# Optimization experiments

Measured on AMD Instinct MI355X. Metric: run time of the kernel, lower is better.

The kernel has to match this reference:

```python
import jax, jax.numpy as jnp
import numpy as np

B, C, IMG, P = 64, 3, 224, 16
GRID = IMG // P          # 14
N = GRID * GRID          # 196 patch tokens
D = 768
L, H = 12, 12
HD = D // H              # 64
FF = 4 * D               # 3072
NC = 1000
PRUNE_LAYER = 6
KEEP = max(1, int(N * 0.5))  # 98 tokens kept after pruning
LN_EPS = 1e-6


def _ln(x, g, b):
    m = jnp.mean(x, axis=-1, keepdims=True)
    v = jnp.var(x, axis=-1, keepdims=True)
    return (x - m) * jax.lax.rsqrt(v + LN_EPS) * g + b


def _block(x, g1, b1, qw, qb, pw, pb, g2, b2, w1, c1, w2, c2):
    # standard timm ViT block: x + Attn(LN(x)); x + MLP(LN(x))
    Bq, S, _ = x.shape
    h = _ln(x, g1, b1)
    qkv = (h @ qw + qb).reshape(Bq, S, 3, H, HD)
    q, k, v = qkv[:, :, 0], qkv[:, :, 1], qkv[:, :, 2]  # [B,S,H,HD]
    attn = jax.nn.softmax(jnp.einsum('bqhd,bkhd->bhqk', q, k) * (HD ** -0.5), axis=-1)
    o = jnp.einsum('bhqk,bkhd->bqhd', attn, v).reshape(Bq, S, D)
    x = x + o @ pw + pb
    h = _ln(x, g2, b2)
    return x + jax.nn.gelu(h @ w1 + c1, approximate=False) @ w2 + c2


def _forward(x, patch_w, patch_b, cls_token, pos_embed, ln1_g, ln1_b, qkv_w, qkv_b,
             proj_w, proj_b, ln2_g, ln2_b, fc1_w, fc1_b, fc2_w, fc2_b,
             norm_g, norm_b, head_w, head_b):
    Bq = x.shape[0]
    # patch embed: conv(k=16, s=16) == patchify + linear; flatten order (C, ph, pw) matches torch conv weight layout
    patches = x.reshape(Bq, C, GRID, P, GRID, P).transpose(0, 2, 4, 1, 3, 5).reshape(Bq, N, C * P * P)
    t = patches @ patch_w + patch_b                                     # [B,N,D]
    t = jnp.concatenate([jnp.broadcast_to(cls_token, (Bq, 1, D)), t], axis=1) + pos_embed  # [B,197,D]

    blk = lambda t, i: _block(t, ln1_g[i], ln1_b[i], qkv_w[i], qkv_b[i], proj_w[i], proj_b[i],
                              ln2_g[i], ln2_b[i], fc1_w[i], fc1_b[i], fc2_w[i], fc2_b[i])
    for i in range(PRUNE_LAYER):
        t = blk(t, i)

    cls_tok, patch_tok = t[:, :1], t[:, 1:]
    # per-token L2 scores + topk selection + gather (the irregular-access stage)
    scores = jnp.sqrt(jnp.sum(patch_tok * patch_tok, axis=-1))          # [B,N]
    _, idx = jax.lax.top_k(scores, KEEP)                                # sorted descending, matches torch.topk
    sel = jnp.take_along_axis(patch_tok, idx[:, :, None], axis=1)       # [B,K,D]
    t = jnp.concatenate([cls_tok, sel], axis=1)                         # [B,K+1,D]

    for i in range(PRUNE_LAYER, L):
        t = blk(t, i)
    t = _ln(t, norm_g, norm_b)
    return t[:, 0] @ head_w + head_b                                    # [B,NC]


def setup_inputs() -> dict:
    key = jax.random.key(0)
    ks = jax.random.split(key, 12)
    s = 0.02
    f32 = jnp.float32
    return {
        'x': jax.random.normal(ks[0], (B, C, IMG, IMG), f32),
        'patch_w': jax.random.normal(ks[1], (C * P * P, D), f32) * s,
        'patch_b': jnp.zeros((D,), f32),
        'cls_token': jax.random.normal(ks[2], (1, 1, D), f32) * s,
        'pos_embed': jax.random.normal(ks[3], (1, N + 1, D), f32) * s,
        'ln1_g': jnp.ones((L, D), f32), 'ln1_b': jnp.zeros((L, D), f32),
        'qkv_w': jax.random.normal(ks[4], (L, D, 3 * D), f32) * s,
        'qkv_b': jnp.zeros((L, 3 * D), f32),
        'proj_w': jax.random.normal(ks[5], (L, D, D), f32) * s,
        'proj_b': jnp.zeros((L, D), f32),
        'ln2_g': jnp.ones((L, D), f32), 'ln2_b': jnp.zeros((L, D), f32),
        'fc1_w': jax.random.normal(ks[6], (L, D, FF), f32) * s,
        'fc1_b': jnp.zeros((L, FF), f32),
        'fc2_w': jax.random.normal(ks[7], (L, FF, D), f32) * s,
        'fc2_b': jnp.zeros((L, D), f32),
        'norm_g': jnp.ones((D,), f32), 'norm_b': jnp.zeros((D,), f32),
        'head_w': jax.random.normal(ks[8], (D, NC), f32) * s,
        'head_b': jnp.zeros((NC,), f32),
    }


def reference(x, patch_w, patch_b, cls_token, pos_embed, ln1_g, ln1_b, qkv_w, qkv_b,
              proj_w, proj_b, ln2_g, ln2_b, fc1_w, fc1_b, fc2_w, fc2_b,
              norm_g, norm_b, head_w, head_b):
    return _forward(x, patch_w, patch_b, cls_token, pos_embed, ln1_g, ln1_b, qkv_w, qkv_b,
                    proj_w, proj_b, ln2_g, ln2_b, fc1_w, fc1_b, fc2_w, fc2_b,
                    norm_g, norm_b, head_w, head_b)
```

## Files before the change

kernel.cpp:

```cpp
#include <hip/hip_runtime.h>
#include <hip/hip_bf16.h>
#include <cstddef>
#include <cstdint>

namespace {

constexpr int B = 64, CIN = 3, IMG = 224, PS = 16, GRID_ = 14, NPATCH = 196;
constexpr int D = 768, H = 12, HD = 64, FFD = 3072, NC = 1000;
constexpr int S1 = 197, S2 = 99, KEEP = 98, PRUNE = 6, LAYERS = 12;
constexpr float LN_EPS = 1e-6f;

typedef __attribute__((ext_vector_type(8))) short bf16x8;
typedef __attribute__((ext_vector_type(4))) float f32x4;

__device__ inline float wave_red_sum(float v) {
  #pragma unroll
  for (int off = 32; off > 0; off >>= 1) v += __shfl_xor(v, off, 64);
  return v;
}

__device__ inline void gl16(const __hip_bfloat16* g, __hip_bfloat16* l) {
  __builtin_amdgcn_global_load_lds(
      (const __attribute__((address_space(1))) void*)g,
      (__attribute__((address_space(3))) void*)l,
      16, 0, 0);
}

__global__ __launch_bounds__(256) void tcvt_k(const float* __restrict__ src,
                                              __hip_bfloat16* __restrict__ dst,
                                              int R, int C, size_t lstride) {
  src += (size_t)blockIdx.z * lstride;
  dst += (size_t)blockIdx.z * lstride;
  __shared__ float tile[32][33];
  int c0 = blockIdx.x * 32, r0 = blockIdx.y * 32;
  int tx = threadIdx.x & 31, ty = threadIdx.x >> 5;
  #pragma unroll
  for (int i = 0; i < 32; i += 8) {
    int r = r0 + ty + i, c = c0 + tx;
    tile[ty + i][tx] = (r < R && c < C) ? src[(size_t)r * C + c] : 0.f;
  }
  __syncthreads();
  #pragma unroll
  for (int i = 0; i < 32; i += 8) {
    int c = c0 + ty + i, r = r0 + tx;
    if (c < C && r < R) dst[(size_t)c * R + r] = __float2bfloat16(tile[tx][ty + i]);
  }
}

__global__ void patchify_k(const float* __restrict__ x, __hip_bfloat16* __restrict__ out) {
  size_t idx = (size_t)blockIdx.x * blockDim.x + threadIdx.x;
  size_t total = (size_t)B * NPATCH * D;
  if (idx >= total) return;
  int row = (int)(idx / D), k = (int)(idx % D);
  int b = row / NPATCH, n = row % NPATCH;
  int gr = n / GRID_, gc = n % GRID_;
  int c = k / (PS * PS), rr = (k % (PS * PS)) / PS, cc = k % PS;
  out[idx] = __float2bfloat16(x[((size_t)(b * CIN + c) * IMG + (gr * PS + rr)) * IMG + gc * PS + cc]);
}

template <int MODE, int KC>
__global__ __launch_bounds__(256) void bgemm_k(
    const __hip_bfloat16* __restrict__ A, const __hip_bfloat16* __restrict__ BT,
    const float* __restrict__ bias, void* __restrict__ Cc,
    int M, int N, const float* __restrict__ extra) {
  __shared__ __hip_bfloat16 As[3][128 * 32];
  __shared__ __hip_bfloat16 Bs[3][128 * 32];
  int tid = threadIdx.x, lane = tid & 63, wv = tid >> 6;
  int wr = wv >> 1, wc = wv & 1;

  int nbx = gridDim.x, nby = gridDim.y;
  int nwg = nbx * nby;
  int flat = blockIdx.y * nbx + blockIdx.x;
  int q8 = nwg >> 3, r8 = nwg & 7;
  int xcd = flat & 7, pos = flat >> 3;
  int nf = (xcd < r8 ? xcd * (q8 + 1) : r8 * (q8 + 1) + (xcd - r8) * q8) + pos;
  constexpr int G = 8;
  int fullS = nby / G, tailR = nby - fullS * G;
  int fullCount = fullS * G * nbx;
  int bx, by;
  if (nf < fullCount) {
    int sup = nf / (G * nbx);
    int rem = nf - sup * G * nbx;
    bx = rem / G;
    by = sup * G + (rem - bx * G);
  } else {
    int rem = nf - fullCount;
    bx = rem / tailR;
    by = fullS * G + (rem - bx * tailR);
  }
  int m0 = by * 128, n0 = bx * 128;

  int fr = lane & 15, fq = lane >> 4;
  int srow = lane >> 2;
  int scd = (lane & 3) ^ ((lane >> 3) & 3);
  int rswz = (fq ^ ((fr >> 1) & 3)) * 8;
  constexpr int NK = KC >> 5;

  int r0i = m0 + wv * 32 + srow, r1i = r0i + 16;
  int ga0 = (r0i < M) ? r0i : (M - 1), ga1 = (r1i < M) ? r1i : (M - 1);
  int c0i = n0 + wv * 32 + srow, c1i = c0i + 16;
  int gb0 = (c0i < N) ? c0i : (N - 1), gb1 = (c1i < N) ? c1i : (N - 1);
  const __hip_bfloat16* pa0 = A + (size_t)ga0 * KC + scd * 8;
  const __hip_bfloat16* pa1 = A + (size_t)ga1 * KC + scd * 8;
  const __hip_bfloat16* pb0 = BT + (size_t)gb0 * KC + scd * 8;
  const __hip_bfloat16* pb1 = BT + (size_t)gb1 * KC + scd * 8;

  auto stage = [&](int buf, int kt) {
    int ko = kt << 5;
    gl16(pa0 + ko, &As[buf][(wv * 32) * 32]);
    gl16(pa1 + ko, &As[buf][(wv * 32 + 16) * 32]);
    gl16(pb0 + ko, &Bs[buf][(wv * 32) * 32]);
    gl16(pb1 + ko, &Bs[buf][(wv * 32 + 16) * 32]);
  };

  f32x4 acc[4][4] = {};
  stage(0, 0);
  stage(1, 1);
  #pragma unroll 4
  for (int kt = 0; kt < NK; ++kt) {
    int buf = kt % 3;
    if (kt + 2 < NK) {
      stage((kt + 2) % 3, kt + 2);
      asm volatile("s_waitcnt vmcnt(8)" ::: "memory");
    } else if (kt + 1 < NK) {
      asm volatile("s_waitcnt vmcnt(4)" ::: "memory");
    } else {
      asm volatile("s_waitcnt vmcnt(0)" ::: "memory");
    }
    asm volatile("s_barrier" ::: "memory");
    bf16x8 af[4], bg[4];
    #pragma unroll
    for (int m = 0; m < 4; ++m)
      af[m] = *(const bf16x8*)&As[buf][(wr * 64 + m * 16 + fr) * 32 + rswz];
    #pragma unroll
    for (int n = 0; n < 4; ++n)
      bg[n] = *(const bf16x8*)&Bs[buf][(wc * 64 + n * 16 + fr) * 32 + rswz];
    #pragma unroll
    for (int m = 0; m < 4; ++m)
      #pragma unroll
      for (int n = 0; n < 4; ++n)
        acc[m][n] = __builtin_amdgcn_mfma_f32_16x16x32_bf16(af[m], bg[n], acc[m][n], 0, 0, 0);
    asm volatile("s_waitcnt lgkmcnt(0)" ::: "memory");
    asm volatile("s_barrier" ::: "memory");
  }
  #pragma unroll
  for (int m = 0; m < 4; ++m) {
    #pragma unroll
    for (int n = 0; n < 4; ++n) {
      #pragma unroll
      for (int j = 0; j < 4; ++j) {
        int row = m0 + wr * 64 + m * 16 + fq * 4 + j;
        int col = n0 + wc * 64 + n * 16 + fr;
        if (row >= M || col >= N) continue;
        float v = acc[m][n][j] + bias[col];
        if (MODE == 0) {
          ((__hip_bfloat16*)Cc)[(size_t)row * N + col] = __float2bfloat16(v);
        } else if (MODE == 1) {
          int b = row / NPATCH, nn = row % NPATCH;
          ((float*)Cc)[((size_t)(b * S1 + 1 + nn)) * D + col] = v + extra[(size_t)(1 + nn) * D + col];
        } else if (MODE == 2) {
          ((float*)Cc)[(size_t)row * N + col] += v;
        } else {
          float g = 0.5f * v * (1.0f + erff(v * 0.7071067811865476f));
          ((__hip_bfloat16*)Cc)[(size_t)row * N + col] = __float2bfloat16(g);
        }
      }
    }
  }
}

__global__ __launch_bounds__(256) void gemm_k(
    const float* __restrict__ A, const float* __restrict__ Bw,
    const float* __restrict__ bias, float* __restrict__ Cc,
    int M, int N, int K) {
  __shared__ float As[64][17];
  __shared__ float Bs[16][64];
  int tid = threadIdx.x;
  int tx = tid & 15, ty = tid >> 4;
  int m0 = blockIdx.y * 64, n0 = blockIdx.x * 64;
  float acc[4][4] = {};
  for (int k0 = 0; k0 < K; k0 += 16) {
    #pragma unroll
    for (int j = 0; j < 4; ++j) {
      int i = tid + 256 * j;
      int r = i >> 4, c = i & 15;
      int gr = m0 + r;
      As[r][c] = (gr < M) ? A[(size_t)gr * K + (k0 + c)] : 0.f;
    }
    #pragma unroll
    for (int j = 0; j < 4; ++j) {
      int i = tid + 256 * j;
      int r = i >> 6, c = i & 63;
      int gc = n0 + c;
      Bs[r][c] = (gc < N) ? Bw[(size_t)(k0 + r) * N + gc] : 0.f;
    }
    __syncthreads();
    #pragma unroll
    for (int kk = 0; kk < 16; ++kk) {
      float a[4], bb[4];
      #pragma unroll
      for (int ii = 0; ii < 4; ++ii) a[ii] = As[ty * 4 + ii][kk];
      #pragma unroll
      for (int jj = 0; jj < 4; ++jj) bb[jj] = Bs[kk][tx * 4 + jj];
      #pragma unroll
      for (int ii = 0; ii < 4; ++ii)
        #pragma unroll
        for (int jj = 0; jj < 4; ++jj) acc[ii][jj] = fmaf(a[ii], bb[jj], acc[ii][jj]);
    }
    __syncthreads();
  }
  #pragma unroll
  for (int ii = 0; ii < 4; ++ii) {
    int row = m0 + ty * 4 + ii;
    if (row >= M) continue;
    #pragma unroll
    for (int jj = 0; jj < 4; ++jj) {
      int col = n0 + tx * 4 + jj;
      if (col >= N) continue;
      Cc[(size_t)row * N + col] = acc[ii][jj] + bias[col];
    }
  }
}

__global__ void cls_init_k(float* __restrict__ t, const float* __restrict__ cls,
                           const float* __restrict__ pos) {
  int idx = blockIdx.x * blockDim.x + threadIdx.x;
  if (idx >= B * D) return;
  int b = idx / D, d = idx % D;
  t[(size_t)b * S1 * D + d] = cls[d] + pos[d];
}

template <typename OutT>
__global__ __launch_bounds__(192) void ln_k(const float* __restrict__ in, OutT* __restrict__ out,
                                            const float* __restrict__ g, const float* __restrict__ bta,
                                            size_t istride, size_t ostride) {
  int row = blockIdx.x, tid = threadIdx.x;
  const float4* p = (const float4*)(in + (size_t)row * istride);
  float4 v = p[tid];
  float s = v.x + v.y + v.z + v.w;
  float s2 = v.x * v.x + v.y * v.y + v.z * v.z + v.w * v.w;
  s = wave_red_sum(s);
  s2 = wave_red_sum(s2);
  __shared__ float r1[3], r2[3];
  int lane = tid & 63, w = tid >> 6;
  if (lane == 0) { r1[w] = s; r2[w] = s2; }
  __syncthreads();
  s = r1[0] + r1[1] + r1[2];
  s2 = r2[0] + r2[1] + r2[2];
  float mean = s * (1.0f / 768.0f);
  float var = s2 * (1.0f / 768.0f) - mean * mean;
  float rs = rsqrtf(var + LN_EPS);
  float4 gv = ((const float4*)g)[tid];
  float4 bv = ((const float4*)bta)[tid];
  float o0 = (v.x - mean) * rs * gv.x + bv.x;
  float o1 = (v.y - mean) * rs * gv.y + bv.y;
  float o2 = (v.z - mean) * rs * gv.z + bv.z;
  float o3 = (v.w - mean) * rs * gv.w + bv.w;
  if constexpr (sizeof(OutT) == 2) {
    __hip_bfloat16 hb[4] = {__float2bfloat16(o0), __float2bfloat16(o1),
                            __float2bfloat16(o2), __float2bfloat16(o3)};
    *(uint2*)((__hip_bfloat16*)out + (size_t)row * ostride + tid * 4) = *(uint2*)hb;
  } else {
    ((float4*)((float*)out + (size_t)row * ostride))[tid] = make_float4(o0, o1, o2, o3);
  }
}

template <int NT16>
__global__ __launch_bounds__(256) void attn3_k(const __hip_bfloat16* __restrict__ qkv,
                                               __hip_bfloat16* __restrict__ o, int S) {
  constexpr int NT32 = (NT16 + 1) / 2;
  constexpr int COLS = NT32 * 32;
  constexpr int STR = COLS + 8;
  __shared__ __hip_bfloat16 VT[64 * STR];
  __shared__ __hip_bfloat16 P[4][16 * STR];
  int bh = blockIdx.x;
  int b = bh / H, hh = bh % H;
  int tid = threadIdx.x, lane = tid & 63, wv = tid >> 6;
  int fr = lane & 15, fq = lane >> 4;
  const size_t rs = 3 * D;
  const __hip_bfloat16* qb = qkv + ((size_t)b * S) * rs + hh * HD;
  const __hip_bfloat16* kb = qb + D;
  const __hip_bfloat16* vb = qb + 2 * D;
  const __hip_bfloat16 z = __float2bfloat16(0.f);
  for (int idx = tid; idx < COLS * 64; idx += 256) {
    int key = idx >> 6, d = idx & 63;
    VT[d * STR + key] = (key < S) ? vb[(size_t)key * rs + d] : z;
  }
  if (NT16 & 1) {
    for (int idx = lane; idx < 16 * 16; idx += 64)
      P[wv][(idx >> 4) * STR + NT16 * 16 + (idx & 15)] = z;
  }
  __syncthreads();

  for (int qt = wv; qt * 16 < S; qt += 4) {
    int q0 = qt * 16;
    int qrow = q0 + fr;
    const __hip_bfloat16* qp = qb + (size_t)(qrow < S ? qrow : 0) * rs + fq * 8;
    bf16x8 aq0 = *(const bf16x8*)(qp);
    bf16x8 aq1 = *(const bf16x8*)(qp + 32);
    f32x4 sc[NT16];
    #pragma unroll
    for (int kt = 0; kt < NT16; ++kt) {
      int krow = kt * 16 + fr;
      const __hip_bfloat16* kp = kb + (size_t)(krow < S ? krow : 0) * rs + fq * 8;
      bf16x8 bk0 = *(const bf16x8*)(kp);
      bf16x8 bk1 = *(const bf16x8*)(kp + 32);
      f32x4 a = {};
      a = __builtin_amdgcn_mfma_f32_16x16x32_bf16(aq0, bk0, a, 0, 0, 0);
      a = __builtin_amdgcn_mfma_f32_16x16x32_bf16(aq1, bk1, a, 0, 0, 0);
      sc[kt] = a;
    }
    float lj[4];
    #pragma unroll
    for (int jj = 0; jj < 4; ++jj) {
      float mx = -1e30f;
      #pragma unroll
      for (int kt = 0; kt < NT16; ++kt) {
        float v = sc[kt][jj] * 0.125f;
        if (kt * 16 + fr >= S) v = -1e30f;
        sc[kt][jj] = v;
        mx = fmaxf(mx, v);
      }
      mx = fmaxf(mx, __shfl_xor(mx, 1, 64));
      mx = fmaxf(mx, __shfl_xor(mx, 2, 64));
      mx = fmaxf(mx, __shfl_xor(mx, 4, 64));
      mx = fmaxf(mx, __shfl_xor(mx, 8, 64));
      float sum = 0.f;
      #pragma unroll
      for (int kt = 0; kt < NT16; ++kt) {
        float p = __expf(sc[kt][jj] - mx);
        sc[kt][jj] = p;
        sum += p;
      }
      sum += __shfl_xor(sum, 1, 64);
      sum += __shfl_xor(sum, 2, 64);
      sum += __shfl_xor(sum, 4, 64);
      sum += __shfl_xor(sum, 8, 64);
      lj[jj] = 1.0f / sum;
    }
    __hip_bfloat16* pw = &P[wv][0];
    #pragma unroll
    for (int kt = 0; kt < NT16; ++kt)
      #pragma unroll
      for (int jj = 0; jj < 4; ++jj)
        pw[(fq * 4 + jj) * STR + kt * 16 + fr] = __float2bfloat16(sc[kt][jj]);
    #pragma unroll
    for (int dt = 0; dt < 4; ++dt) {
      f32x4 oa = {};
      #pragma unroll
      for (int kc = 0; kc < NT32; ++kc) {
        bf16x8 ap = *(const bf16x8*)&pw[fr * STR + kc * 32 + fq * 8];
        bf16x8 bv = *(const bf16x8*)&VT[(dt * 16 + fr) * STR + kc * 32 + fq * 8];
        oa = __builtin_amdgcn_mfma_f32_16x16x32_bf16(ap, bv, oa, 0, 0, 0);
      }
      #pragma unroll
      for (int jj = 0; jj < 4; ++jj) {
        int orow = q0 + fq * 4 + jj;
        if (orow < S)
          o[((size_t)(b * S + orow)) * D + hh * HD + dt * 16 + fr] =
              __float2bfloat16(oa[jj] * lj[jj]);
      }
    }
  }
}

__global__ void score_k(const float* __restrict__ t, float* __restrict__ scores) {
  int gw = (blockIdx.x * blockDim.x + threadIdx.x) >> 6;
  int lane = threadIdx.x & 63;
  if (gw >= B * NPATCH) return;
  int b = gw / NPATCH, n = gw % NPATCH;
  const float* p = t + ((size_t)(b * S1) + 1 + n) * D;
  float a = 0.f;
  #pragma unroll
  for (int j = lane; j < D; j += 64) { float v = p[j]; a += v * v; }
  a = wave_red_sum(a);
  if (lane == 0) scores[gw] = sqrtf(a);
}

__global__ __launch_bounds__(256) void select_k(const float* __restrict__ scores, int* __restrict__ map) {
  int b = blockIdx.x;
  __shared__ float s[NPATCH];
  __shared__ int flag[NPATCH];
  int i = threadIdx.x;
  if (i < NPATCH) s[i] = scores[b * NPATCH + i];
  __syncthreads();
  if (i < NPATCH) {
    float si = s[i];
    int r = 0;
    for (int j = 0; j < NPATCH; ++j) {
      float sj = s[j];
      r += (sj > si) || (sj == si && j < i);
    }
    flag[i] = (r < KEEP) ? 1 : 0;
  }
  __syncthreads();
  if (i < NPATCH && flag[i]) {
    int p = 0;
    for (int j = 0; j < i; ++j) p += flag[j];
    map[b * (KEEP + 1) + 1 + p] = 1 + i;
  }
  if (i == 0) map[b * (KEEP + 1)] = 0;
}

__global__ void gather_k(const float* __restrict__ t, const int* __restrict__ map,
                         float* __restrict__ t2) {
  int br = blockIdx.x;
  int b = br / S2;
  int src = map[br];
  const float* p = t + ((size_t)b * S1 + src) * D;
  float* q = t2 + (size_t)br * D;
  for (int j = threadIdx.x; j < D; j += blockDim.x) q[j] = p[j];
}

}

extern "C" void kernel_launch(void* const* d_in, const int* in_sizes, int n_in,
                              void* d_out, int out_size, void* d_ws, size_t ws_size,
                              hipStream_t stream) {
  const float* x       = (const float*)d_in[0];
  const float* patch_w = (const float*)d_in[1];
  const float* patch_b = (const float*)d_in[2];
  const float* cls_tok = (const float*)d_in[3];
  const float* pos_emb = (const float*)d_in[4];
  const float* ln1_g   = (const float*)d_in[5];
  const float* ln1_b   = (const float*)d_in[6];
  const float* qkv_w   = (const float*)d_in[7];
  const float* qkv_b   = (const float*)d_in[8];
  const float* proj_w  = (const float*)d_in[9];
  const float* proj_b  = (const float*)d_in[10];
  const float* ln2_g   = (const float*)d_in[11];
  const float* ln2_b   = (const float*)d_in[12];
  const float* fc1_w   = (const float*)d_in[13];
  const float* fc1_b   = (const float*)d_in[14];
  const float* fc2_w   = (const float*)d_in[15];
  const float* fc2_b   = (const float*)d_in[16];
  const float* norm_g  = (const float*)d_in[17];
  const float* norm_b  = (const float*)d_in[18];
  const float* head_w  = (const float*)d_in[19];
  const float* head_b  = (const float*)d_in[20];
  float* out = (float*)d_out;

  char* wp = (char*)d_ws;
  auto alloc = [&](size_t bytes) { char* r = wp; wp += (bytes + 255) & ~(size_t)255; return r; };
  float* t   = (float*)alloc((size_t)B * S1 * D * 4);
  float* t2  = (float*)alloc((size_t)B * S2 * D * 4);
  float* hf  = (float*)alloc((size_t)B * D * 4);
  float* scores = (float*)alloc((size_t)B * NPATCH * 4);
  int*   map    = (int*)alloc((size_t)B * S2 * 4);
  __hip_bfloat16* h   = (__hip_bfloat16*)alloc((size_t)B * S1 * D * 2);
  __hip_bfloat16* qkv = (__hip_bfloat16*)alloc((size_t)B * S1 * 3 * D * 2);
  __hip_bfloat16* ff  = (__hip_bfloat16*)alloc((size_t)B * S1 * FFD * 2);
  __hip_bfloat16* qkvT  = (__hip_bfloat16*)alloc((size_t)LAYERS * 3 * D * D * 2);
  __hip_bfloat16* projT = (__hip_bfloat16*)alloc((size_t)LAYERS * D * D * 2);
  __hip_bfloat16* fc1T  = (__hip_bfloat16*)alloc((size_t)LAYERS * FFD * D * 2);
  __hip_bfloat16* fc2T  = (__hip_bfloat16*)alloc((size_t)LAYERS * D * FFD * 2);
  __hip_bfloat16* patchT = (__hip_bfloat16*)alloc((size_t)D * D * 2);
  __hip_bfloat16* patches = ff;

  { dim3 g(3 * D / 32, D / 32, LAYERS);
    tcvt_k<<<g, 256, 0, stream>>>(qkv_w, qkvT, D, 3 * D, (size_t)D * 3 * D); }
  { dim3 g(D / 32, D / 32, LAYERS);
    tcvt_k<<<g, 256, 0, stream>>>(proj_w, projT, D, D, (size_t)D * D); }
  { dim3 g(FFD / 32, D / 32, LAYERS);
    tcvt_k<<<g, 256, 0, stream>>>(fc1_w, fc1T, D, FFD, (size_t)D * FFD); }
  { dim3 g(D / 32, FFD / 32, LAYERS);
    tcvt_k<<<g, 256, 0, stream>>>(fc2_w, fc2T, FFD, D, (size_t)FFD * D); }
  { dim3 g(D / 32, D / 32, 1);
    tcvt_k<<<g, 256, 0, stream>>>(patch_w, patchT, D, D, 0); }

  {
    size_t total = (size_t)B * NPATCH * D;
    patchify_k<<<(unsigned)((total + 255) / 256), 256, 0, stream>>>(x, patches);
    dim3 g(D / 128, (B * NPATCH) / 128);
    bgemm_k<1, 768><<<g, 256, 0, stream>>>(patches, patchT, patch_b, t, B * NPATCH, D, pos_emb);
    cls_init_k<<<(B * D + 255) / 256, 256, 0, stream>>>(t, cls_tok, pos_emb);
  }

  auto run_block = [&](float* tb, int S, int l) {
    int M = B * S;
    int mb = (M + 127) / 128;
    ln_k<__hip_bfloat16><<<M, 192, 0, stream>>>(tb, h, ln1_g + (size_t)l * D, ln1_b + (size_t)l * D, D, D);
    { dim3 g(3 * D / 128, mb);
      bgemm_k<0, 768><<<g, 256, 0, stream>>>(h, qkvT + (size_t)l * 3 * D * D, qkv_b + (size_t)l * 3 * D,
                                             qkv, M, 3 * D, nullptr); }
    if (S == S1) attn3_k<13><<<B * H, 256, 0, stream>>>(qkv, h, S);
    else         attn3_k<7><<<B * H, 256, 0, stream>>>(qkv, h, S);
    { dim3 g(D / 128, mb);
      bgemm_k<2, 768><<<g, 256, 0, stream>>>(h, projT + (size_t)l * D * D, proj_b + (size_t)l * D,
                                             tb, M, D, nullptr); }
    ln_k<__hip_bfloat16><<<M, 192, 0, stream>>>(tb, h, ln2_g + (size_t)l * D, ln2_b + (size_t)l * D, D, D);
    { dim3 g(FFD / 128, mb);
      bgemm_k<3, 768><<<g, 256, 0, stream>>>(h, fc1T + (size_t)l * FFD * D, fc1_b + (size_t)l * FFD,
                                             ff, M, FFD, nullptr); }
    { dim3 g(D / 128, mb);
      bgemm_k<2, 3072><<<g, 256, 0, stream>>>(ff, fc2T + (size_t)l * D * FFD, fc2_b + (size_t)l * D,
                                              tb, M, D, nullptr); }
  };

  for (int l = 0; l < PRUNE; ++l) run_block(t, S1, l);

  score_k<<<(B * NPATCH * 64 + 255) / 256, 256, 0, stream>>>(t, scores);
  select_k<<<B, 256, 0, stream>>>(scores, map);
  gather_k<<<B * S2, 256, 0, stream>>>(t, map, t2);

  for (int l = PRUNE; l < LAYERS; ++l) run_block(t2, S2, l);

  ln_k<float><<<B, 192, 0, stream>>>(t2, hf, norm_g, norm_b, (size_t)S2 * D, D);
  { dim3 g((NC + 63) / 64, (B + 63) / 64);
    gemm_k<<<g, 256, 0, stream>>>(hf, head_w, head_b, out, B, NC, D); }
}
```

Before: 5.778 ms.

## Add 64-row GEMM tile variant for narrow-N GEMMs and drop XCD swizzle

Templates the bf16 MFMA GEMM on the M tile height (128 or 64) and uses 64-row tiles for the proj GEMM and the post-prune fc2 GEMM, where N=768 gives only six column tiles. The smaller tile doubles the workgroup count to fill more CUs, at the cost of less B-tile reuse per workgroup. It also removes the XCD-aware grouped block remapping, which can hurt L2 locality, and drops the unroll-4 pragma on the k loop.

```diff
diff --git a/kernel.cpp b/kernel.cpp
--- a/kernel.cpp
+++ b/kernel.cpp
@@ -58,85 +58,74 @@
   out[idx] = __float2bfloat16(x[((size_t)(b * CIN + c) * IMG + (gr * PS + rr)) * IMG + gc * PS + cc]);
 }
 
-template <int MODE, int KC>
+template <int MODE, int KC, int BM>
 __global__ __launch_bounds__(256) void bgemm_k(
     const __hip_bfloat16* __restrict__ A, const __hip_bfloat16* __restrict__ BT,
     const float* __restrict__ bias, void* __restrict__ Cc,
     int M, int N, const float* __restrict__ extra) {
-  __shared__ __hip_bfloat16 As[3][128 * 32];
+  constexpr int MR = BM / 32;
+  __shared__ __hip_bfloat16 As[3][BM * 32];
   __shared__ __hip_bfloat16 Bs[3][128 * 32];
   int tid = threadIdx.x, lane = tid & 63, wv = tid >> 6;
   int wr = wv >> 1, wc = wv & 1;
-
-  int nbx = gridDim.x, nby = gridDim.y;
-  int nwg = nbx * nby;
-  int flat = blockIdx.y * nbx + blockIdx.x;
-  int q8 = nwg >> 3, r8 = nwg & 7;
-  int xcd = flat & 7, pos = flat >> 3;
-  int nf = (xcd < r8 ? xcd * (q8 + 1) : r8 * (q8 + 1) + (xcd - r8) * q8) + pos;
-  constexpr int G = 8;
-  int fullS = nby / G, tailR = nby - fullS * G;
-  int fullCount = fullS * G * nbx;
-  int bx, by;
-  if (nf < fullCount) {
-    int sup = nf / (G * nbx);
-    int rem = nf - sup * G * nbx;
-    bx = rem / G;
-    by = sup * G + (rem - bx * G);
-  } else {
-    int rem = nf - fullCount;
-    bx = rem / tailR;
-    by = fullS * G + (rem - bx * tailR);
-  }
-  int m0 = by * 128, n0 = bx * 128;
-
+  int m0 = blockIdx.y * BM, n0 = blockIdx.x * 128;
   int fr = lane & 15, fq = lane >> 4;
   int srow = lane >> 2;
   int scd = (lane & 3) ^ ((lane >> 3) & 3);
   int rswz = (fq ^ ((fr >> 1) & 3)) * 8;
   constexpr int NK = KC >> 5;
 
-  int r0i = m0 + wv * 32 + srow, r1i = r0i + 16;
-  int ga0 = (r0i < M) ? r0i : (M - 1), ga1 = (r1i < M) ? r1i : (M - 1);
-  int c0i = n0 + wv * 32 + srow, c1i = c0i + 16;
-  int gb0 = (c0i < N) ? c0i : (N - 1), gb1 = (c1i < N) ? c1i : (N - 1);
+  int ar0 = m0 + (BM == 128 ? wv * 32 : wv * 16) + srow;
+  int ga0 = (ar0 < M) ? ar0 : (M - 1);
   const __hip_bfloat16* pa0 = A + (size_t)ga0 * KC + scd * 8;
-  const __hip_bfloat16* pa1 = A + (size_t)ga1 * KC + scd * 8;
+  const __hip_bfloat16* pa1 = pa0;
+  if constexpr (BM == 128) {
+    int ar1 = ar0 + 16;
+    int ga1 = (ar1 < M) ? ar1 : (M - 1);
+    pa1 = A + (size_t)ga1 * KC + scd * 8;
+  }
+  int br0 = n0 + wv * 32 + srow, br1 = br0 + 16;
+  int gb0 = (br0 < N) ? br0 : (N - 1), gb1 = (br1 < N) ? br1 : (N - 1);
   const __hip_bfloat16* pb0 = BT + (size_t)gb0 * KC + scd * 8;
   const __hip_bfloat16* pb1 = BT + (size_t)gb1 * KC + scd * 8;
 
   auto stage = [&](int buf, int kt) {
     int ko = kt << 5;
-    gl16(pa0 + ko, &As[buf][(wv * 32) * 32]);
-    gl16(pa1 + ko, &As[buf][(wv * 32 + 16) * 32]);
+    if constexpr (BM == 128) {
+      gl16(pa0 + ko, &As[buf][(wv * 32) * 32]);
+      gl16(pa1 + ko, &As[buf][(wv * 32 + 16) * 32]);
+    } else {
+      gl16(pa0 + ko, &As[buf][(wv * 16) * 32]);
+    }
     gl16(pb0 + ko, &Bs[buf][(wv * 32) * 32]);
     gl16(pb1 + ko, &Bs[buf][(wv * 32 + 16) * 32]);
   };
 
-  f32x4 acc[4][4] = {};
+  f32x4 acc[MR][4] = {};
   stage(0, 0);
   stage(1, 1);
-  #pragma unroll 4
   for (int kt = 0; kt < NK; ++kt) {
     int buf = kt % 3;
     if (kt + 2 < NK) {
       stage((kt + 2) % 3, kt + 2);
-      asm volatile("s_waitcnt vmcnt(8)" ::: "memory");
+      if constexpr (BM == 128) asm volatile("s_waitcnt vmcnt(8)" ::: "memory");
+      else                     asm volatile("s_waitcnt vmcnt(6)" ::: "memory");
     } else if (kt + 1 < NK) {
-      asm volatile("s_waitcnt vmcnt(4)" ::: "memory");
+      if constexpr (BM == 128) asm volatile("s_waitcnt vmcnt(4)" ::: "memory");
+      else                     asm volatile("s_waitcnt vmcnt(3)" ::: "memory");
     } else {
       asm volatile("s_waitcnt vmcnt(0)" ::: "memory");
     }
     asm volatile("s_barrier" ::: "memory");
-    bf16x8 af[4], bg[4];
-    #pragma unroll
-    for (int m = 0; m < 4; ++m)
-      af[m] = *(const bf16x8*)&As[buf][(wr * 64 + m * 16 + fr) * 32 + rswz];
+    bf16x8 af[MR], bg[4];
+    #pragma unroll
+    for (int m = 0; m < MR; ++m)
+      af[m] = *(const bf16x8*)&As[buf][(wr * (BM / 2) + m * 16 + fr) * 32 + rswz];
     #pragma unroll
     for (int n = 0; n < 4; ++n)
       bg[n] = *(const bf16x8*)&Bs[buf][(wc * 64 + n * 16 + fr) * 32 + rswz];
     #pragma unroll
-    for (int m = 0; m < 4; ++m)
+    for (int m = 0; m < MR; ++m)
       #pragma unroll
       for (int n = 0; n < 4; ++n)
         acc[m][n] = __builtin_amdgcn_mfma_f32_16x16x32_bf16(af[m], bg[n], acc[m][n], 0, 0, 0);
@@ -144,12 +133,12 @@
     asm volatile("s_barrier" ::: "memory");
   }
   #pragma unroll
-  for (int m = 0; m < 4; ++m) {
+  for (int m = 0; m < MR; ++m) {
     #pragma unroll
     for (int n = 0; n < 4; ++n) {
       #pragma unroll
       for (int j = 0; j < 4; ++j) {
-        int row = m0 + wr * 64 + m * 16 + fq * 4 + j;
+        int row = m0 + wr * (BM / 2) + m * 16 + fq * 4 + j;
         int col = n0 + wc * 64 + n * 16 + fr;
         if (row >= M || col >= N) continue;
         float v = acc[m][n][j] + bias[col];
@@ -472,29 +461,36 @@
     size_t total = (size_t)B * NPATCH * D;
     patchify_k<<<(unsigned)((total + 255) / 256), 256, 0, stream>>>(x, patches);
     dim3 g(D / 128, (B * NPATCH) / 128);
-    bgemm_k<1, 768><<<g, 256, 0, stream>>>(patches, patchT, patch_b, t, B * NPATCH, D, pos_emb);
+    bgemm_k<1, 768, 128><<<g, 256, 0, stream>>>(patches, patchT, patch_b, t, B * NPATCH, D, pos_emb);
     cls_init_k<<<(B * D + 255) / 256, 256, 0, stream>>>(t, cls_tok, pos_emb);
   }
 
   auto run_block = [&](float* tb, int S, int l) {
     int M = B * S;
-    int mb = (M + 127) / 128;
+    int mb128 = (M + 127) / 128;
+    int mb64 = (M + 63) / 64;
     ln_k<__hip_bfloat16><<<M, 192, 0, stream>>>(tb, h, ln1_g + (size_t)l * D, ln1_b + (size_t)l * D, D, D);
-    { dim3 g(3 * D / 128, mb);
-      bgemm_k<0, 768><<<g, 256, 0, stream>>>(h, qkvT + (size_t)l * 3 * D * D, qkv_b + (size_t)l * 3 * D,
-                                             qkv, M, 3 * D, nullptr); }
+    { dim3 g(3 * D / 128, mb128);
+      bgemm_k<0, 768, 128><<<g, 256, 0, stream>>>(h, qkvT + (size_t)l * 3 * D * D, qkv_b + (size_t)l * 3 * D,
+                                                  qkv, M, 3 * D, nullptr); }
     if (S == S1) attn3_k<13><<<B * H, 256, 0, stream>>>(qkv, h, S);
     else         attn3_k<7><<<B * H, 256, 0, stream>>>(qkv, h, S);
-    { dim3 g(D / 128, mb);
-      bgemm_k<2, 768><<<g, 256, 0, stream>>>(h, projT + (size_t)l * D * D, proj_b + (size_t)l * D,
-                                             tb, M, D, nullptr); }
+    { dim3 g(D / 128, mb64);
+      bgemm_k<2, 768, 64><<<g, 256, 0, stream>>>(h, projT + (size_t)l * D * D, proj_b + (size_t)l * D,
+                                                 tb, M, D, nullptr); }
     ln_k<__hip_bfloat16><<<M, 192, 0, stream>>>(tb, h, ln2_g + (size_t)l * D, ln2_b + (size_t)l * D, D, D);
-    { dim3 g(FFD / 128, mb);
-      bgemm_k<3, 768><<<g, 256, 0, stream>>>(h, fc1T + (size_t)l * FFD * D, fc1_b + (size_t)l * FFD,
-                                             ff, M, FFD, nullptr); }
-    { dim3 g(D / 128, mb);
-      bgemm_k<2, 3072><<<g, 256, 0, stream>>>(ff, fc2T + (size_t)l * D * FFD, fc2_b + (size_t)l * D,
-                                              tb, M, D, nullptr); }
+    { dim3 g(FFD / 128, mb128);
+      bgemm_k<3, 768, 128><<<g, 256, 0, stream>>>(h, fc1T + (size_t)l * FFD * D, fc1_b + (size_t)l * FFD,
+                                                  ff, M, FFD, nullptr); }
+    if (S == S1) {
+      dim3 g(D / 128, mb128);
+      bgemm_k<2, 3072, 128><<<g, 256, 0, stream>>>(ff, fc2T + (size_t)l * D * FFD, fc2_b + (size_t)l * D,
+                                                   tb, M, D, nullptr);
+    } else {
+      dim3 g(D / 128, mb64);
+      bgemm_k<2, 3072, 64><<<g, 256, 0, stream>>>(ff, fc2T + (size_t)l * D * FFD, fc2_b + (size_t)l * D,
+                                                  tb, M, D, nullptr);
+    }
   };
 
   for (int l = 0; l < PRUNE; ++l) run_block(t, S1, l);
```

Result: faster. 5.010 ms (-13.3%).
